# Kernel optimization log

Measured on AMD Instinct MI355X. Metric: run time of the kernel, lower is better.

Reference implementation:

```python
import jax, jax.numpy as jnp
import numpy as np

B, P, H, A = 256, 196, 1024, 512

def setup_inputs() -> dict:
    key = jax.random.key(0)
    ks = jax.random.split(key, 20)
    s = 1.0 / np.sqrt(H)
    sa = 1.0 / np.sqrt(A)
    return {
        "spatial_image": jax.random.normal(ks[0], (B, P, H), jnp.float32),
        "decoder_out": jax.random.normal(ks[1], (B, H), jnp.float32),
        "st": jax.random.normal(ks[2], (B, H), jnp.float32),
        "W_sen_aff": jax.random.uniform(ks[3], (H, H), jnp.float32, -s, s),
        "b_sen_aff": jax.random.uniform(ks[4], (H,), jnp.float32, -s, s),
        "W_sen_att": jax.random.uniform(ks[5], (H, A), jnp.float32, -s, s),
        "b_sen_att": jax.random.uniform(ks[6], (A,), jnp.float32, -s, s),
        "W_h_aff": jax.random.uniform(ks[7], (H, H), jnp.float32, -s, s),
        "b_h_aff": jax.random.uniform(ks[8], (H,), jnp.float32, -s, s),
        "W_h_att": jax.random.uniform(ks[9], (H, A), jnp.float32, -s, s),
        "b_h_att": jax.random.uniform(ks[10], (A,), jnp.float32, -s, s),
        "W_v_att": jax.random.uniform(ks[11], (H, A), jnp.float32, -s, s),
        "b_v_att": jax.random.uniform(ks[12], (A,), jnp.float32, -s, s),
        "W_alpha": jax.random.uniform(ks[13], (A, 1), jnp.float32, -sa, sa),
        "b_alpha": jax.random.uniform(ks[14], (1,), jnp.float32, -sa, sa),
        "W_ctx": jax.random.uniform(ks[15], (H, H), jnp.float32, -s, s),
        "b_ctx": jax.random.uniform(ks[16], (H,), jnp.float32, -s, s),
    }

def reference(spatial_image, decoder_out, st,
              W_sen_aff, b_sen_aff, W_sen_att, b_sen_att,
              W_h_aff, b_h_aff, W_h_att, b_h_att,
              W_v_att, b_v_att, W_alpha, b_alpha, W_ctx, b_ctx):
    # visual_attn: [B, P, A]
    visual_attn = jnp.einsum('bph,ha->bpa', spatial_image, W_v_att) + b_v_att
    # sentinel path: [B, H] -> relu affine -> [B, A]
    sentinel_affine = jax.nn.relu(st @ W_sen_aff + b_sen_aff)
    sentinel_attn = sentinel_affine @ W_sen_att + b_sen_att
    # hidden path: [B, H] -> tanh affine -> [B, A]
    hidden_affine = jnp.tanh(decoder_out @ W_h_aff + b_h_aff)
    hidden_attn = hidden_affine @ W_h_att + b_h_att
    # concat sentinel as an extra "pixel": [B, P+1, H] and [B, P+1, A]
    concat_features = jnp.concatenate([spatial_image, sentinel_affine[:, None, :]], axis=1)
    attended_features = jnp.concatenate([visual_attn, sentinel_attn[:, None, :]], axis=1)
    attention = jnp.tanh(attended_features + hidden_attn[:, None, :])  # [B, P+1, A]
    alpha = (jnp.einsum('bpa,ao->bpo', attention, W_alpha) + b_alpha)[..., 0]  # [B, P+1]
    att_weights = jax.nn.softmax(alpha, axis=1)
    context = jnp.einsum('bph,bp->bh', concat_features, att_weights)  # [B, H]
    beta_value = att_weights[:, -1:]  # [B, 1]
    out_l = jnp.tanh((context + hidden_affine) @ W_ctx + b_ctx)  # [B, H]
    return (out_l, att_weights, beta_value)
```

## Files before the change

### kernel.cpp

```cpp
#include <hip/hip_runtime.h>
#include <hip/hip_bf16.h>
#include <stdint.h>
#include <stddef.h>

typedef __attribute__((ext_vector_type(4))) float f32x4;
typedef __attribute__((ext_vector_type(8))) short short8;

#define MROWS 50176


static __device__ __forceinline__ int lds_off(int row, int k) {
    int slot = (k >> 3) ^ ((row >> 1) & 3);
    return (row << 6) + (slot << 4) + ((k & 7) << 1);
}

static __device__ __forceinline__ unsigned div196(unsigned g) {
    return (unsigned)(((unsigned long long)g * 85599ull) >> 24);
}

static __device__ __forceinline__ unsigned short f2bf(float f) {
    union { float f; unsigned u; } v; v.f = f;
    unsigned r = v.u + 0x7FFFu + ((v.u >> 16) & 1u);
    return (unsigned short)(r >> 16);
}

static __device__ __forceinline__ unsigned long long pack4bf(f32x4 a) {
    union { unsigned long long u; __hip_bfloat162 h[2]; } r;
    r.h[0] = __float22bfloat162_rn(make_float2(a[0], a[1]));
    r.h[1] = __float22bfloat162_rn(make_float2(a[2], a[3]));
    return r.u;
}

static __device__ __forceinline__ float tanh_fast(float x) {
    float xc = fminf(fmaxf(x, -9.f), 9.f);
    float e = __builtin_amdgcn_exp2f(xc * 2.885390081777927f);
    return (e - 1.f) * __builtin_amdgcn_rcpf(e + 1.f);
}

static __device__ __forceinline__ void gload_lds16(const void* g, void* l) {
    __builtin_amdgcn_global_load_lds(
        (const __attribute__((address_space(1))) unsigned int*)g,
        (__attribute__((address_space(3))) unsigned int*)l, 16, 0, 0);
}

template<bool PREF, bool LATE, int VEND>
static __device__ __forceinline__ void pipe_step(
    int t,
    const float* const (&Ap)[4], const int (&aoff)[4],
    const unsigned short* const (&Bp)[2], const int (&bdst)[2],
    char* sAcur, char* sAnxt, char* sB, int bc, int bn,
    f32x4 (&aCon)[4], f32x4 (&aFill)[4], f32x4 (&acc)[4][4],
    int wr, int wc, int lrow, int lk)
{
    char* sBc = sB + (bc << 13);
    if (PREF) {
        char* sBn = sB + (bn << 13);
        const int ko = (t + 2) << 5;
        gload_lds16(Bp[0] + ko, sBn + bdst[0]);
        gload_lds16(Bp[1] + ko, sBn + bdst[1]);
        #pragma unroll
        for (int r = 0; r < 4; ++r) aFill[r] = *(const f32x4*)(Ap[r] + ko);
    }
    short8 af[4], bf[4];
    #pragma unroll
    for (int m = 0; m < 4; ++m)
        af[m] = *(const short8*)(sAcur + lds_off((wr << 6) + (m << 4) + lrow, lk << 3));
    #pragma unroll
    for (int n = 0; n < 4; ++n)
        bf[n] = *(const short8*)(sBc + lds_off((wc << 6) + (n << 4) + lrow, lk << 3));
    __builtin_amdgcn_s_setprio(1);
    #pragma unroll
    for (int m = 0; m < 4; ++m)
        #pragma unroll
        for (int n = 0; n < 4; ++n)
            acc[m][n] = __builtin_amdgcn_mfma_f32_16x16x32_bf16(af[m], bf[n], acc[m][n], 0, 0, 0);
    __builtin_amdgcn_s_setprio(0);
    if (LATE) {
        #pragma unroll
        for (int r = 0; r < 4; ++r)
            *(unsigned long long*)(sAnxt + aoff[r]) = pack4bf(aCon[r]);
        asm volatile("s_waitcnt vmcnt(%0)" :: "n"(VEND) : "memory");
        asm volatile("s_waitcnt lgkmcnt(0)" ::: "memory");
        __builtin_amdgcn_s_barrier();
    }
}

static __device__ __forceinline__ void kloop_pipe(
    const float* __restrict__ Abase,
    const unsigned short* __restrict__ Bbase,
    char* sA, char* sB,
    f32x4 (&acc)[4][4], int tid)
{
    const int lane = tid & 63, w = tid >> 6;
    const int lrow = lane & 15, lk = lane >> 4;
    const int wr = w >> 1, wc = w & 1;

    const float* Ap[4];
    int aoff[4];
    #pragma unroll
    for (int r = 0; r < 4; ++r) {
        int q = tid + (r << 8);
        int ar = q >> 3, kc = (q & 7) << 2;
        Ap[r] = Abase + (size_t)ar * 1024 + kc;
        aoff[r] = lds_off(ar, kc);
    }
    const unsigned short* Bp[2];
    int bdst[2];
    #pragma unroll
    for (int c = 0; c < 2; ++c) {
        int ch = (w << 1) + c;
        int row = (ch << 4) + (lane >> 2);
        int kg = (lane & 3) ^ ((row >> 1) & 3);
        Bp[c] = Bbase + (size_t)row * 1024 + (kg << 3);
        bdst[c] = ch << 10;
    }

    f32x4 z = {0.f, 0.f, 0.f, 0.f};
    #pragma unroll
    for (int m = 0; m < 4; ++m)
        #pragma unroll
        for (int n = 0; n < 4; ++n) acc[m][n] = z;

    f32x4 aX[4], aY[4];

    gload_lds16(Bp[0], sB + bdst[0]);
    gload_lds16(Bp[1], sB + bdst[1]);
    gload_lds16(Bp[0] + 32, sB + 8192 + bdst[0]);
    gload_lds16(Bp[1] + 32, sB + 8192 + bdst[1]);
    #pragma unroll
    for (int r = 0; r < 4; ++r) aX[r] = *(const f32x4*)Ap[r];
    asm volatile("s_waitcnt vmcnt(0)" ::: "memory");
    #pragma unroll
    for (int r = 0; r < 4; ++r)
        *(unsigned long long*)(sA + aoff[r]) = pack4bf(aX[r]);
    #pragma unroll
    for (int r = 0; r < 4; ++r) aY[r] = *(const f32x4*)(Ap[r] + 32);
    asm volatile("s_waitcnt lgkmcnt(0)" ::: "memory");
    __builtin_amdgcn_s_barrier();

    int bc = 0, bn = 2;
    #pragma unroll 1
    for (int t = 0; t < 30; t += 2) {
        pipe_step<true, true, 6>(t, Ap, aoff, Bp, bdst,
            sA, sA + 8192, sB, bc, bn, aY, aX, acc, wr, wc, lrow, lk);
        bc = (bc == 2) ? 0 : bc + 1;  bn = (bn == 2) ? 0 : bn + 1;
        pipe_step<true, true, 6>(t + 1, Ap, aoff, Bp, bdst,
            sA + 8192, sA, sB, bc, bn, aX, aY, acc, wr, wc, lrow, lk);
        bc = (bc == 2) ? 0 : bc + 1;  bn = (bn == 2) ? 0 : bn + 1;
    }
    pipe_step<false, true, 0>(30, Ap, aoff, Bp, bdst,
        sA, sA + 8192, sB, bc, bn, aY, aX, acc, wr, wc, lrow, lk);
    bc = (bc == 2) ? 0 : bc + 1;
    pipe_step<false, false, 0>(31, Ap, aoff, Bp, bdst,
        sA + 8192, sA, sB, bc, bn, aX, aY, acc, wr, wc, lrow, lk);
}

__global__ __launch_bounds__(256, 3) void attn_alpha_kernel(
    const float* __restrict__ spatial,
    const unsigned short* __restrict__ WvT,
    const float* __restrict__ b_v_att,
    const float* __restrict__ hidden_attn,
    const float* __restrict__ W_alpha,
    float* __restrict__ alphap)
{
    __shared__ char sA[2][8192];
    __shared__ char sB[3][8192];
    __shared__ float alpha_s[2][128];
    const int tid = threadIdx.x;
    const int j = blockIdx.x;
    const int wk = (j & 7) * 196 + (j >> 3);
    const int mt = wk >> 2, n4 = wk & 3;
    const int row0 = mt << 7, col0 = n4 << 7;

    f32x4 acc[4][4];
    kloop_pipe(spatial + (size_t)row0 * 1024, WvT + (size_t)col0 * 1024,
               &sA[0][0], &sB[0][0], acc, tid);

    const int lane = tid & 63, w = tid >> 6;
    const int wr = w >> 1, wc = w & 1;
    const int lrow = lane & 15, lk = lane >> 4;

    const unsigned bb0 = div196((unsigned)row0);
    const unsigned bb1 = div196((unsigned)(row0 + 127));
    float bv[4], wa[4], h0[4], h1[4];
    #pragma unroll
    for (int n = 0; n < 4; ++n) {
        int g = col0 + (wc << 6) + (n << 4) + lrow;
        bv[n] = b_v_att[g];
        wa[n] = W_alpha[g];
        h0[n] = hidden_attn[bb0 * 512 + g];
        h1[n] = hidden_attn[bb1 * 512 + g];
    }
    #pragma unroll
    for (int m = 0; m < 4; ++m) {
        #pragma unroll
        for (int i = 0; i < 4; ++i) {
            int rloc = (wr << 6) + (m << 4) + (lk << 2) + i;
            bool first = (div196((unsigned)(row0 + rloc)) == bb0);
            float s = 0.f;
            #pragma unroll
            for (int n = 0; n < 4; ++n) {
                float v = tanh_fast(acc[m][n][i] + bv[n] + (first ? h0[n] : h1[n]));
                s += v * wa[n];
            }
            #pragma unroll
            for (int off = 1; off < 16; off <<= 1) s += __shfl_xor(s, off);
            if (lrow == 0) alpha_s[wc][rloc] = s;
        }
    }
    __syncthreads();
    if (tid < 128)
        alphap[(size_t)n4 * MROWS + row0 + tid] = alpha_s[0][tid] + alpha_s[1][tid];
}

static __device__ __forceinline__ void kloop_dbuf(
    const float* __restrict__ Abase,
    const unsigned short* __restrict__ Bbase,
    char* sA0, char* sA1, char* sB0, char* sB1,
    f32x4 acc[4][4], int tid)
{
    const int lane = tid & 63, w = tid >> 6;
    const int lrow = lane & 15, lk = lane >> 4;
    const int wr = w >> 1, wc = w & 1;

    const float* Ap[4];
    int aoff[4];
    #pragma unroll
    for (int r = 0; r < 4; ++r) {
        int q = tid + (r << 8);
        int ar = q >> 3, kc = (q & 7) << 2;
        Ap[r] = Abase + (size_t)ar * 1024 + kc;
        aoff[r] = lds_off(ar, kc);
    }
    const unsigned short* Bp[2];
    int bdst[2];
    #pragma unroll
    for (int c = 0; c < 2; ++c) {
        int ch = (w << 1) + c;
        int row = (ch << 4) + (lane >> 2);
        int kg = (lane & 3) ^ ((row >> 1) & 3);
        Bp[c] = Bbase + (size_t)row * 1024 + (kg << 3);
        bdst[c] = ch << 10;
    }

    f32x4 z = {0.f, 0.f, 0.f, 0.f};
    #pragma unroll
    for (int m = 0; m < 4; ++m)
        #pragma unroll
        for (int n = 0; n < 4; ++n) acc[m][n] = z;

    {
        f32x4 a[4];
        #pragma unroll
        for (int r = 0; r < 4; ++r) a[r] = *(const f32x4*)Ap[r];
        #pragma unroll
        for (int c = 0; c < 2; ++c) gload_lds16(Bp[c], sB0 + bdst[c]);
        #pragma unroll
        for (int r = 0; r < 4; ++r)
            *(unsigned long long*)(sA0 + aoff[r]) = pack4bf(a[r]);
    }
    __syncthreads();

    char* sAc = sA0; char* sAn = sA1;
    char* sBc = sB0; char* sBn = sB1;
    for (int ks = 0; ks < 32; ++ks) {
        f32x4 an[4];
        if (ks < 31) {
            const int ko = (ks + 1) << 5;
            #pragma unroll
            for (int r = 0; r < 4; ++r) an[r] = *(const f32x4*)(Ap[r] + ko);
            #pragma unroll
            for (int c = 0; c < 2; ++c) gload_lds16(Bp[c] + ko, sBn + bdst[c]);
        }
        short8 af[4], bf[4];
        #pragma unroll
        for (int m = 0; m < 4; ++m)
            af[m] = *(const short8*)(sAc + lds_off((wr << 6) + (m << 4) + lrow, lk << 3));
        #pragma unroll
        for (int n = 0; n < 4; ++n)
            bf[n] = *(const short8*)(sBc + lds_off((wc << 6) + (n << 4) + lrow, lk << 3));
        #pragma unroll
        for (int m = 0; m < 4; ++m)
            #pragma unroll
            for (int n = 0; n < 4; ++n)
                acc[m][n] = __builtin_amdgcn_mfma_f32_16x16x32_bf16(af[m], bf[n], acc[m][n], 0, 0, 0);
        if (ks < 31) {
            #pragma unroll
            for (int r = 0; r < 4; ++r)
                *(unsigned long long*)(sAn + aoff[r]) = pack4bf(an[r]);
        }
        __syncthreads();
        char* t;
        t = sAc; sAc = sAn; sAn = t;
        t = sBc; sBc = sBn; sBn = t;
    }
}

struct GemmDesc { const float* A; const unsigned short* BT; const float* bias; float* C; int N; int act; };
struct GemmPair { GemmDesc d[2]; };

__global__ __launch_bounds__(256, 4) void gemm_pair_kernel(GemmPair p)
{
    GemmDesc d = p.d[blockIdx.z];
    __shared__ char sA[2][8192];
    __shared__ char sB[2][8192];
    const int tid = threadIdx.x;
    const int row0 = blockIdx.x << 7;
    const int col0 = blockIdx.y << 7;
    f32x4 acc[4][4];
    kloop_dbuf(d.A + (size_t)row0 * 1024, d.BT + (size_t)col0 * 1024,
               sA[0], sA[1], sB[0], sB[1], acc, tid);
    const int lane = tid & 63, w = tid >> 6;
    const int wr = w >> 1, wc = w & 1;
    const int lrow = lane & 15, lk = lane >> 4;
    #pragma unroll
    for (int n = 0; n < 4; ++n) {
        int col = col0 + (wc << 6) + (n << 4) + lrow;
        float bs = d.bias[col];
        #pragma unroll
        for (int m = 0; m < 4; ++m) {
            int rbase = row0 + (wr << 6) + (m << 4) + (lk << 2);
            #pragma unroll
            for (int i = 0; i < 4; ++i) {
                float v = acc[m][n][i] + bs;
                if (d.act == 1) v = fmaxf(v, 0.f);
                if (d.act == 2) v = tanh_fast(v);
                d.C[(size_t)(rbase + i) * d.N + col] = v;
            }
        }
    }
}

struct TransDesc { const float* src; unsigned short* dst; int K; int N; };
struct TransArgs { TransDesc d[6]; };

__global__ void transpose_cvt_kernel(TransArgs args) {
    TransDesc d = args.d[blockIdx.y];
    int nt = d.N >> 5;
    int tiles = (d.K >> 5) * nt;
    if ((int)blockIdx.x >= tiles) return;
    int tk = blockIdx.x / nt, tn = blockIdx.x % nt;
    __shared__ unsigned short tile[32][33];
    int tx = threadIdx.x & 31, ty = threadIdx.x >> 5;
    int k0 = tk << 5, n0 = tn << 5;
    #pragma unroll
    for (int j = 0; j < 4; ++j)
        tile[ty + j * 8][tx] = f2bf(d.src[(size_t)(k0 + ty + j * 8) * d.N + n0 + tx]);
    __syncthreads();
    #pragma unroll
    for (int j = 0; j < 4; ++j)
        d.dst[(size_t)(n0 + ty + j * 8) * d.K + k0 + tx] = tile[tx][ty + j * 8];
}

__global__ void softmax_sentinel_kernel(
    const float* __restrict__ alphap,
    const float* __restrict__ sen_att, const float* __restrict__ hid_att,
    const float* __restrict__ W_alpha,
    float* __restrict__ att, float* __restrict__ beta)
{
    int b = blockIdx.x, tid = threadIdx.x;
    __shared__ float al[197];
    __shared__ float red[4];
    if (tid < 196) {
        size_t g = (size_t)b * 196 + tid;
        al[tid] = alphap[g] + alphap[MROWS + g] + alphap[2 * MROWS + g] + alphap[3 * MROWS + g];
    }
    float s = 0.f;
    for (int a = tid; a < 512; a += 256)
        s += tanh_fast(sen_att[b * 512 + a] + hid_att[b * 512 + a]) * W_alpha[a];
    #pragma unroll
    for (int off = 1; off < 64; off <<= 1) s += __shfl_xor(s, off);
    if ((tid & 63) == 0) red[tid >> 6] = s;
    __syncthreads();
    if (tid == 0) al[196] = red[0] + red[1] + red[2] + red[3];
    __syncthreads();
    if (tid < 64) {
        float v[4];
        float mx = -1e30f;
        #pragma unroll
        for (int jj = 0; jj < 4; ++jj) {
            int i = tid + jj * 64;
            v[jj] = (i < 197) ? al[i] : -1e30f;
            mx = fmaxf(mx, v[jj]);
        }
        #pragma unroll
        for (int off = 1; off < 64; off <<= 1) mx = fmaxf(mx, __shfl_xor(mx, off));
        float sm = 0.f;
        #pragma unroll
        for (int jj = 0; jj < 4; ++jj) {
            v[jj] = __builtin_amdgcn_exp2f((v[jj] - mx) * 1.442695040888963f);
            if (tid + jj * 64 >= 197) v[jj] = 0.f;
            sm += v[jj];
        }
        #pragma unroll
        for (int off = 1; off < 64; off <<= 1) sm += __shfl_xor(sm, off);
        float inv = 1.f / sm;
        #pragma unroll
        for (int jj = 0; jj < 4; ++jj) {
            int i = tid + jj * 64;
            if (i < 197) {
                float wv = v[jj] * inv;
                att[b * 197 + i] = wv;
                if (i == 196) beta[b] = wv;
            }
        }
    }
}

__global__ __launch_bounds__(256) void context_kernel(
    const float* __restrict__ spatial, const float* __restrict__ sen_aff,
    const float* __restrict__ hid_aff, const float* __restrict__ att,
    float* __restrict__ ctxh)
{
    int b = blockIdx.x, half = blockIdx.y, t = threadIdx.x;
    __shared__ float wsm[197];
    if (t < 197) wsm[t] = att[b * 197 + t];
    __syncthreads();
    int h2 = (half << 8) + t;
    const float2* sp = (const float2*)(spatial + (size_t)b * 196 * 1024) + h2;
    float ax = 0.f, ay = 0.f;
    #pragma unroll 8
    for (int p = 0; p < 196; ++p) {
        float2 x = sp[(size_t)p * 512];
        ax += wsm[p] * x.x; ay += wsm[p] * x.y;
    }
    float w196 = wsm[196];
    float2 sa = ((const float2*)(sen_aff + (size_t)b * 1024))[h2];
    float2 ha = ((const float2*)(hid_aff + (size_t)b * 1024))[h2];
    ctxh[(size_t)b * 1024 + 2 * h2]     = ax + w196 * sa.x + ha.x;
    ctxh[(size_t)b * 1024 + 2 * h2 + 1] = ay + w196 * sa.y + ha.y;
}

extern "C" void kernel_launch(void* const* d_in, const int* in_sizes, int n_in,
                              void* d_out, int out_size, void* d_ws, size_t ws_size,
                              hipStream_t stream)
{
    const float* spatial   = (const float*)d_in[0];
    const float* decoder   = (const float*)d_in[1];
    const float* st        = (const float*)d_in[2];
    const float* W_sen_aff = (const float*)d_in[3];
    const float* b_sen_aff = (const float*)d_in[4];
    const float* W_sen_att = (const float*)d_in[5];
    const float* b_sen_att = (const float*)d_in[6];
    const float* W_h_aff   = (const float*)d_in[7];
    const float* b_h_aff   = (const float*)d_in[8];
    const float* W_h_att   = (const float*)d_in[9];
    const float* b_h_att   = (const float*)d_in[10];
    const float* W_v_att   = (const float*)d_in[11];
    const float* b_v_att   = (const float*)d_in[12];
    const float* W_alpha   = (const float*)d_in[13];
    const float* W_ctx     = (const float*)d_in[15];
    const float* b_ctx     = (const float*)d_in[16];

    char* ws = (char*)d_ws;
    size_t off = 0;
    auto alloc = [&](size_t bytes) {
        char* p = ws + off; off += (bytes + 255) & ~(size_t)255; return p;
    };
    unsigned short* WvT  = (unsigned short*)alloc((size_t)512 * 1024 * 2);
    unsigned short* WsaT = (unsigned short*)alloc((size_t)1024 * 1024 * 2);
    unsigned short* WstT = (unsigned short*)alloc((size_t)512 * 1024 * 2);
    unsigned short* WhaT = (unsigned short*)alloc((size_t)1024 * 1024 * 2);
    unsigned short* WhtT = (unsigned short*)alloc((size_t)512 * 1024 * 2);
    unsigned short* WcxT = (unsigned short*)alloc((size_t)1024 * 1024 * 2);
    float* sen_aff = (float*)alloc((size_t)256 * 1024 * 4);
    float* sen_att = (float*)alloc((size_t)256 * 512 * 4);
    float* hid_aff = (float*)alloc((size_t)256 * 1024 * 4);
    float* hid_att = (float*)alloc((size_t)256 * 512 * 4);
    float* alphap  = (float*)alloc((size_t)4 * MROWS * 4);
    float* ctxh    = (float*)alloc((size_t)256 * 1024 * 4);

    float* out_l    = (float*)d_out;
    float* out_att  = out_l + 256 * 1024;
    float* out_beta = out_att + 256 * 197;

    TransArgs ta;
    ta.d[0] = { W_v_att,   WvT,  1024, 512  };
    ta.d[1] = { W_sen_aff, WsaT, 1024, 1024 };
    ta.d[2] = { W_sen_att, WstT, 1024, 512  };
    ta.d[3] = { W_h_aff,   WhaT, 1024, 1024 };
    ta.d[4] = { W_h_att,   WhtT, 1024, 512  };
    ta.d[5] = { W_ctx,     WcxT, 1024, 1024 };
    transpose_cvt_kernel<<<dim3(1024, 6), 256, 0, stream>>>(ta);

    GemmPair p1;
    p1.d[0] = { st,      WsaT, b_sen_aff, sen_aff, 1024, 1 };
    p1.d[1] = { decoder, WhaT, b_h_aff,   hid_aff, 1024, 2 };
    gemm_pair_kernel<<<dim3(2, 8, 2), 256, 0, stream>>>(p1);

    GemmPair p2;
    p2.d[0] = { sen_aff, WstT, b_sen_att, sen_att, 512, 0 };
    p2.d[1] = { hid_aff, WhtT, b_h_att,   hid_att, 512, 0 };
    gemm_pair_kernel<<<dim3(2, 4, 2), 256, 0, stream>>>(p2);

    attn_alpha_kernel<<<1568, 256, 0, stream>>>(spatial, WvT, b_v_att, hid_att, W_alpha, alphap);
    softmax_sentinel_kernel<<<256, 256, 0, stream>>>(alphap, sen_att, hid_att, W_alpha, out_att, out_beta);
    context_kernel<<<dim3(256, 2), 256, 0, stream>>>(spatial, sen_aff, hid_aff, out_att, ctxh);

    GemmPair p3;
    p3.d[0] = { ctxh, WcxT, b_ctx, out_l, 1024, 2 };
    p3.d[1] = { ctxh, WcxT, b_ctx, out_l, 1024, 2 };
    gemm_pair_kernel<<<dim3(2, 8, 1), 256, 0, stream>>>(p3);
}
```

Baseline: 224.6 us.

## Pre-convert spatial features to bf16 and reuse them in attention and context

Adds a kernel that converts the whole fp32 spatial tensor to bf16 once. The attention-alpha GEMM then streams both operands straight into LDS with direct global-to-LDS loads in a triple-buffered loop, and the context reduction reads the half-size bf16 copy. It also moves the small GEMMs onto the pipelined K-loop. The extra conversion pass reads the full fp32 tensor and writes a bf16 copy, which costs about as much traffic as the single fp32 read it replaces. The context sum now uses bf16-rounded spatial values, and the path is chosen only when the workspace is large enough.

Result: slower. 400.6 us (+78.4%).

```diff
diff --git a/kernel.cpp b/kernel.cpp
--- a/kernel.cpp
+++ b/kernel.cpp
@@ -22,6 +22,10 @@
     union { float f; unsigned u; } v; v.f = f;
     unsigned r = v.u + 0x7FFFu + ((v.u >> 16) & 1u);
     return (unsigned short)(r >> 16);
+}
+
+static __device__ __forceinline__ float bf2f(unsigned short u) {
+    union { unsigned v; float f; } x; x.v = ((unsigned)u) << 16; return x.f;
 }
 
 static __device__ __forceinline__ unsigned long long pack4bf(f32x4 a) {
@@ -43,50 +47,24 @@
         (__attribute__((address_space(3))) unsigned int*)l, 16, 0, 0);
 }
 
-template<bool PREF, bool LATE, int VEND>
-static __device__ __forceinline__ void pipe_step(
-    int t,
-    const float* const (&Ap)[4], const int (&aoff)[4],
-    const unsigned short* const (&Bp)[2], const int (&bdst)[2],
-    char* sAcur, char* sAnxt, char* sB, int bc, int bn,
-    f32x4 (&aCon)[4], f32x4 (&aFill)[4], f32x4 (&acc)[4][4],
-    int wr, int wc, int lrow, int lk)
-{
-    char* sBc = sB + (bc << 13);
-    if (PREF) {
-        char* sBn = sB + (bn << 13);
-        const int ko = (t + 2) << 5;
-        gload_lds16(Bp[0] + ko, sBn + bdst[0]);
-        gload_lds16(Bp[1] + ko, sBn + bdst[1]);
-        #pragma unroll
-        for (int r = 0; r < 4; ++r) aFill[r] = *(const f32x4*)(Ap[r] + ko);
-    }
-    short8 af[4], bf[4];
-    #pragma unroll
-    for (int m = 0; m < 4; ++m)
-        af[m] = *(const short8*)(sAcur + lds_off((wr << 6) + (m << 4) + lrow, lk << 3));
-    #pragma unroll
-    for (int n = 0; n < 4; ++n)
-        bf[n] = *(const short8*)(sBc + lds_off((wc << 6) + (n << 4) + lrow, lk << 3));
-    __builtin_amdgcn_s_setprio(1);
-    #pragma unroll
-    for (int m = 0; m < 4; ++m)
-        #pragma unroll
-        for (int n = 0; n < 4; ++n)
-            acc[m][n] = __builtin_amdgcn_mfma_f32_16x16x32_bf16(af[m], bf[n], acc[m][n], 0, 0, 0);
-    __builtin_amdgcn_s_setprio(0);
-    if (LATE) {
-        #pragma unroll
-        for (int r = 0; r < 4; ++r)
-            *(unsigned long long*)(sAnxt + aoff[r]) = pack4bf(aCon[r]);
-        asm volatile("s_waitcnt vmcnt(%0)" :: "n"(VEND) : "memory");
-        asm volatile("s_waitcnt lgkmcnt(0)" ::: "memory");
-        __builtin_amdgcn_s_barrier();
-    }
-}
-
-static __device__ __forceinline__ void kloop_pipe(
-    const float* __restrict__ Abase,
+__global__ __launch_bounds__(256) void cvt_spatial_kernel(
+    const float* __restrict__ src, unsigned short* __restrict__ dst)
+{
+    const size_t total = (size_t)MROWS * 1024;
+    size_t i = ((size_t)blockIdx.x * 256 + threadIdx.x) * 8;
+    const size_t stride = (size_t)gridDim.x * 256 * 8;
+    for (; i < total; i += stride) {
+        f32x4 lo = *(const f32x4*)(src + i);
+        f32x4 hi = *(const f32x4*)(src + i + 4);
+        union { short8 s; unsigned long long u[2]; } o;
+        o.u[0] = pack4bf(lo);
+        o.u[1] = pack4bf(hi);
+        *(short8*)(dst + i) = o.s;
+    }
+}
+
+static __device__ __forceinline__ void kloop_sym(
+    const unsigned short* __restrict__ Abase,
     const unsigned short* __restrict__ Bbase,
     char* sA, char* sB,
     f32x4 (&acc)[4][4], int tid)
@@ -95,24 +73,16 @@
     const int lrow = lane & 15, lk = lane >> 4;
     const int wr = w >> 1, wc = w & 1;
 
-    const float* Ap[4];
-    int aoff[4];
-    #pragma unroll
-    for (int r = 0; r < 4; ++r) {
-        int q = tid + (r << 8);
-        int ar = q >> 3, kc = (q & 7) << 2;
-        Ap[r] = Abase + (size_t)ar * 1024 + kc;
-        aoff[r] = lds_off(ar, kc);
-    }
-    const unsigned short* Bp[2];
-    int bdst[2];
+    const unsigned short *Ap[2], *Bp[2];
+    int dst[2];
     #pragma unroll
     for (int c = 0; c < 2; ++c) {
         int ch = (w << 1) + c;
         int row = (ch << 4) + (lane >> 2);
         int kg = (lane & 3) ^ ((row >> 1) & 3);
+        Ap[c] = Abase + (size_t)row * 1024 + (kg << 3);
         Bp[c] = Bbase + (size_t)row * 1024 + (kg << 3);
-        bdst[c] = ch << 10;
+        dst[c] = ch << 10;
     }
 
     f32x4 z = {0.f, 0.f, 0.f, 0.f};
@@ -121,49 +91,63 @@
         #pragma unroll
         for (int n = 0; n < 4; ++n) acc[m][n] = z;
 
-    f32x4 aX[4], aY[4];
-
-    gload_lds16(Bp[0], sB + bdst[0]);
-    gload_lds16(Bp[1], sB + bdst[1]);
-    gload_lds16(Bp[0] + 32, sB + 8192 + bdst[0]);
-    gload_lds16(Bp[1] + 32, sB + 8192 + bdst[1]);
-    #pragma unroll
-    for (int r = 0; r < 4; ++r) aX[r] = *(const f32x4*)Ap[r];
-    asm volatile("s_waitcnt vmcnt(0)" ::: "memory");
-    #pragma unroll
-    for (int r = 0; r < 4; ++r)
-        *(unsigned long long*)(sA + aoff[r]) = pack4bf(aX[r]);
-    #pragma unroll
-    for (int r = 0; r < 4; ++r) aY[r] = *(const f32x4*)(Ap[r] + 32);
-    asm volatile("s_waitcnt lgkmcnt(0)" ::: "memory");
+    #pragma unroll
+    for (int s = 0; s < 2; ++s) {
+        const int ko = s << 5;
+        gload_lds16(Ap[0] + ko, sA + (s << 13) + dst[0]);
+        gload_lds16(Ap[1] + ko, sA + (s << 13) + dst[1]);
+        gload_lds16(Bp[0] + ko, sB + (s << 13) + dst[0]);
+        gload_lds16(Bp[1] + ko, sB + (s << 13) + dst[1]);
+    }
+    asm volatile("s_waitcnt vmcnt(4)" ::: "memory");
     __builtin_amdgcn_s_barrier();
 
-    int bc = 0, bn = 2;
+    char *a0 = sA, *a1 = sA + 8192, *a2 = sA + 16384;
+    char *b0 = sB, *b1 = sB + 8192, *b2 = sB + 16384;
     #pragma unroll 1
-    for (int t = 0; t < 30; t += 2) {
-        pipe_step<true, true, 6>(t, Ap, aoff, Bp, bdst,
-            sA, sA + 8192, sB, bc, bn, aY, aX, acc, wr, wc, lrow, lk);
-        bc = (bc == 2) ? 0 : bc + 1;  bn = (bn == 2) ? 0 : bn + 1;
-        pipe_step<true, true, 6>(t + 1, Ap, aoff, Bp, bdst,
-            sA + 8192, sA, sB, bc, bn, aX, aY, acc, wr, wc, lrow, lk);
-        bc = (bc == 2) ? 0 : bc + 1;  bn = (bn == 2) ? 0 : bn + 1;
-    }
-    pipe_step<false, true, 0>(30, Ap, aoff, Bp, bdst,
-        sA, sA + 8192, sB, bc, bn, aY, aX, acc, wr, wc, lrow, lk);
-    bc = (bc == 2) ? 0 : bc + 1;
-    pipe_step<false, false, 0>(31, Ap, aoff, Bp, bdst,
-        sA + 8192, sA, sB, bc, bn, aX, aY, acc, wr, wc, lrow, lk);
-}
-
-__global__ __launch_bounds__(256, 3) void attn_alpha_kernel(
-    const float* __restrict__ spatial,
+    for (int t = 0; t < 32; ++t) {
+        if (t < 30) {
+            const int ko = (t + 2) << 5;
+            gload_lds16(Ap[0] + ko, a2 + dst[0]);
+            gload_lds16(Ap[1] + ko, a2 + dst[1]);
+            gload_lds16(Bp[0] + ko, b2 + dst[0]);
+            gload_lds16(Bp[1] + ko, b2 + dst[1]);
+        }
+        short8 af[4], bf[4];
+        #pragma unroll
+        for (int m = 0; m < 4; ++m)
+            af[m] = *(const short8*)(a0 + lds_off((wr << 6) + (m << 4) + lrow, lk << 3));
+        #pragma unroll
+        for (int n = 0; n < 4; ++n)
+            bf[n] = *(const short8*)(b0 + lds_off((wc << 6) + (n << 4) + lrow, lk << 3));
+        __builtin_amdgcn_s_setprio(1);
+        #pragma unroll
+        for (int m = 0; m < 4; ++m)
+            #pragma unroll
+            for (int n = 0; n < 4; ++n)
+                acc[m][n] = __builtin_amdgcn_mfma_f32_16x16x32_bf16(af[m], bf[n], acc[m][n], 0, 0, 0);
+        __builtin_amdgcn_s_setprio(0);
+        if (t < 31) {
+            if (t < 30) asm volatile("s_waitcnt vmcnt(4)" ::: "memory");
+            else        asm volatile("s_waitcnt vmcnt(0)" ::: "memory");
+            asm volatile("s_waitcnt lgkmcnt(0)" ::: "memory");
+            __builtin_amdgcn_s_barrier();
+            char* t0;
+            t0 = a0; a0 = a1; a1 = a2; a2 = t0;
+            t0 = b0; b0 = b1; b1 = b2; b2 = t0;
+        }
+    }
+}
+
+__global__ __launch_bounds__(256, 3) void attn_alpha_bf16_kernel(
+    const unsigned short* __restrict__ spat_bf,
     const unsigned short* __restrict__ WvT,
     const float* __restrict__ b_v_att,
     const float* __restrict__ hidden_attn,
     const float* __restrict__ W_alpha,
     float* __restrict__ alphap)
 {
-    __shared__ char sA[2][8192];
+    __shared__ char sA[3][8192];
     __shared__ char sB[3][8192];
     __shared__ float alpha_s[2][128];
     const int tid = threadIdx.x;
@@ -173,8 +157,8 @@
     const int row0 = mt << 7, col0 = n4 << 7;
 
     f32x4 acc[4][4];
-    kloop_pipe(spatial + (size_t)row0 * 1024, WvT + (size_t)col0 * 1024,
-               &sA[0][0], &sB[0][0], acc, tid);
+    kloop_sym(spat_bf + (size_t)row0 * 1024, WvT + (size_t)col0 * 1024,
+              &sA[0][0], &sB[0][0], acc, tid);
 
     const int lane = tid & 63, w = tid >> 6;
     const int wr = w >> 1, wc = w & 1;
@@ -213,11 +197,53 @@
         alphap[(size_t)n4 * MROWS + row0 + tid] = alpha_s[0][tid] + alpha_s[1][tid];
 }
 
-static __device__ __forceinline__ void kloop_dbuf(
+template<bool PREF, bool LATE, int VEND>
+static __device__ __forceinline__ void pipe_step(
+    int t,
+    const float* const (&Ap)[4], const int (&aoff)[4],
+    const unsigned short* const (&Bp)[2], const int (&bdst)[2],
+    char* sAcur, char* sAnxt, char* sB, int bc, int bn,
+    f32x4 (&aCon)[4], f32x4 (&aFill)[4], f32x4 (&acc)[4][4],
+    int wr, int wc, int lrow, int lk)
+{
+    char* sBc = sB + (bc << 13);
+    if (PREF) {
+        char* sBn = sB + (bn << 13);
+        const int ko = (t + 2) << 5;
+        gload_lds16(Bp[0] + ko, sBn + bdst[0]);
+        gload_lds16(Bp[1] + ko, sBn + bdst[1]);
+        #pragma unroll
+        for (int r = 0; r < 4; ++r) aFill[r] = *(const f32x4*)(Ap[r] + ko);
+    }
+    short8 af[4], bf[4];
+    #pragma unroll
+    for (int m = 0; m < 4; ++m)
+        af[m] = *(const short8*)(sAcur + lds_off((wr << 6) + (m << 4) + lrow, lk << 3));
+    #pragma unroll
+    for (int n = 0; n < 4; ++n)
+        bf[n] = *(const short8*)(sBc + lds_off((wc << 6) + (n << 4) + lrow, lk << 3));
+    __builtin_amdgcn_s_setprio(1);
+    #pragma unroll
+    for (int m = 0; m < 4; ++m)
+        #pragma unroll
+        for (int n = 0; n < 4; ++n)
+            acc[m][n] = __builtin_amdgcn_mfma_f32_16x16x32_bf16(af[m], bf[n], acc[m][n], 0, 0, 0);
+    __builtin_amdgcn_s_setprio(0);
+    if (LATE) {
+        #pragma unroll
+        for (int r = 0; r < 4; ++r)
+            *(unsigned long long*)(sAnxt + aoff[r]) = pack4bf(aCon[r]);
+        asm volatile("s_waitcnt vmcnt(%0)" :: "n"(VEND) : "memory");
+        asm volatile("s_waitcnt lgkmcnt(0)" ::: "memory");
+        __builtin_amdgcn_s_barrier();
+    }
+}
+
+static __device__ __forceinline__ void kloop_pipe(
     const float* __restrict__ Abase,
     const unsigned short* __restrict__ Bbase,
-    char* sA0, char* sA1, char* sB0, char* sB1,
-    f32x4 acc[4][4], int tid)
+    char* sA, char* sB,
+    f32x4 (&acc)[4][4], int tid)
 {
     const int lane = tid & 63, w = tid >> 6;
     const int lrow = lane & 15, lk = lane >> 4;
@@ -249,51 +275,96 @@
         #pragma unroll
         for (int n = 0; n < 4; ++n) acc[m][n] = z;
 
-    {
-        f32x4 a[4];
-        #pragma unroll
-        for (int r = 0; r < 4; ++r) a[r] = *(const f32x4*)Ap[r];
-        #pragma unroll
-        for (int c = 0; c < 2; ++c) gload_lds16(Bp[c], sB0 + bdst[c]);
-        #pragma unroll
-        for (int r = 0; r < 4; ++r)
-            *(unsigned long long*)(sA0 + aoff[r]) = pack4bf(a[r]);
+    f32x4 aX[4], aY[4];
+
+    gload_lds16(Bp[0], sB + bdst[0]);
+    gload_lds16(Bp[1], sB + bdst[1]);
+    gload_lds16(Bp[0] + 32, sB + 8192 + bdst[0]);
+    gload_lds16(Bp[1] + 32, sB + 8192 + bdst[1]);
+    #pragma unroll
+    for (int r = 0; r < 4; ++r) aX[r] = *(const f32x4*)Ap[r];
+    asm volatile("s_waitcnt vmcnt(0)" ::: "memory");
+    #pragma unroll
+    for (int r = 0; r < 4; ++r)
+        *(unsigned long long*)(sA + aoff[r]) = pack4bf(aX[r]);
+    #pragma unroll
+    for (int r = 0; r < 4; ++r) aY[r] = *(const f32x4*)(Ap[r] + 32);
+    asm volatile("s_waitcnt lgkmcnt(0)" ::: "memory");
+    __builtin_amdgcn_s_barrier();
+
+    int bc = 0, bn = 2;
+    #pragma unroll 1
+    for (int t = 0; t < 30; t += 2) {
+        pipe_step<true, true, 6>(t, Ap, aoff, Bp, bdst,
+            sA, sA + 8192, sB, bc, bn, aY, aX, acc, wr, wc, lrow, lk);
+        bc = (bc == 2) ? 0 : bc + 1;  bn = (bn == 2) ? 0 : bn + 1;
+        pipe_step<true, true, 6>(t + 1, Ap, aoff, Bp, bdst,
+            sA + 8192, sA, sB, bc, bn, aX, aY, acc, wr, wc, lrow, lk);
+        bc = (bc == 2) ? 0 : bc + 1;  bn = (bn == 2) ? 0 : bn + 1;
+    }
+    pipe_step<false, true, 0>(30, Ap, aoff, Bp, bdst,
+        sA, sA + 8192, sB, bc, bn, aY, aX, acc, wr, wc, lrow, lk);
+    bc = (bc == 2) ? 0 : bc + 1;
+    pipe_step<false, false, 0>(31, Ap, aoff, Bp, bdst,
+        sA + 8192, sA, sB, bc, bn, aX, aY, acc, wr, wc, lrow, lk);
+}
+
+__global__ __launch_bounds__(256, 3) void attn_alpha_f32_kernel(
+    const float* __restrict__ spatial,
+    const unsigned short* __restrict__ WvT,
+    const float* __restrict__ b_v_att,
+    const float* __restrict__ hidden_attn,
+    const float* __restrict__ W_alpha,
+    float* __restrict__ alphap)
+{
+    __shared__ char sA[2][8192];
+    __shared__ char sB[3][8192];
+    __shared__ float alpha_s[2][128];
+    const int tid = threadIdx.x;
+    const int j = blockIdx.x;
+    const int wk = (j & 7) * 196 + (j >> 3);
+    const int mt = wk >> 2, n4 = wk & 3;
+    const int row0 = mt << 7, col0 = n4 << 7;
+
+    f32x4 acc[4][4];
+    kloop_pipe(spatial + (size_t)row0 * 1024, WvT + (size_t)col0 * 1024,
+               &sA[0][0], &sB[0][0], acc, tid);
+
+    const int lane = tid & 63, w = tid >> 6;
+    const int wr = w >> 1, wc = w & 1;
+    const int lrow = lane & 15, lk = lane >> 4;
+
+    const unsigned bb0 = div196((unsigned)row0);
+    const unsigned bb1 = div196((unsigned)(row0 + 127));
+    float bv[4], wa[4], h0[4], h1[4];
+    #pragma unroll
+    for (int n = 0; n < 4; ++n) {
+        int g = col0 + (wc << 6) + (n << 4) + lrow;
+        bv[n] = b_v_att[g];
+        wa[n] = W_alpha[g];
+        h0[n] = hidden_attn[bb0 * 512 + g];
+        h1[n] = hidden_attn[bb1 * 512 + g];
+    }
+    #pragma unroll
+    for (int m = 0; m < 4; ++m) {
+        #pragma unroll
+        for (int i = 0; i < 4; ++i) {
+            int rloc = (wr << 6) + (m << 4) + (lk << 2) + i;
+            bool first = (div196((unsigned)(row0 + rloc)) == bb0);
+            float s = 0.f;
+            #pragma unroll
+            for (int n = 0; n < 4; ++n) {
+                float v = tanh_fast(acc[m][n][i] + bv[n] + (first ? h0[n] : h1[n]));
+                s += v * wa[n];
+            }
+            #pragma unroll
+            for (int off = 1; off < 16; off <<= 1) s += __shfl_xor(s, off);
+            if (lrow == 0) alpha_s[wc][rloc] = s;
+        }
     }
     __syncthreads();
-
-    char* sAc = sA0; char* sAn = sA1;
-    char* sBc = sB0; char* sBn = sB1;
-    for (int ks = 0; ks < 32; ++ks) {
-        f32x4 an[4];
-        if (ks < 31) {
-            const int ko = (ks + 1) << 5;
-            #pragma unroll
-            for (int r = 0; r < 4; ++r) an[r] = *(const f32x4*)(Ap[r] + ko);
-            #pragma unroll
-            for (int c = 0; c < 2; ++c) gload_lds16(Bp[c] + ko, sBn + bdst[c]);
-        }
-        short8 af[4], bf[4];
-        #pragma unroll
-        for (int m = 0; m < 4; ++m)
-            af[m] = *(const short8*)(sAc + lds_off((wr << 6) + (m << 4) + lrow, lk << 3));
-        #pragma unroll
-        for (int n = 0; n < 4; ++n)
-            bf[n] = *(const short8*)(sBc + lds_off((wc << 6) + (n << 4) + lrow, lk << 3));
-        #pragma unroll
-        for (int m = 0; m < 4; ++m)
-            #pragma unroll
-            for (int n = 0; n < 4; ++n)
-                acc[m][n] = __builtin_amdgcn_mfma_f32_16x16x32_bf16(af[m], bf[n], acc[m][n], 0, 0, 0);
-        if (ks < 31) {
-            #pragma unroll
-            for (int r = 0; r < 4; ++r)
-                *(unsigned long long*)(sAn + aoff[r]) = pack4bf(an[r]);
-        }
-        __syncthreads();
-        char* t;
-        t = sAc; sAc = sAn; sAn = t;
-        t = sBc; sBc = sBn; sBn = t;
-    }
+    if (tid < 128)
+        alphap[(size_t)n4 * MROWS + row0 + tid] = alpha_s[0][tid] + alpha_s[1][tid];
 }
 
 struct GemmDesc { const float* A; const unsigned short* BT; const float* bias; float* C; int N; int act; };
@@ -303,13 +374,13 @@
 {
     GemmDesc d = p.d[blockIdx.z];
     __shared__ char sA[2][8192];
-    __shared__ char sB[2][8192];
+    __shared__ char sB[3][8192];
     const int tid = threadIdx.x;
     const int row0 = blockIdx.x << 7;
     const int col0 = blockIdx.y << 7;
     f32x4 acc[4][4];
-    kloop_dbuf(d.A + (size_t)row0 * 1024, d.BT + (size_t)col0 * 1024,
-               sA[0], sA[1], sB[0], sB[1], acc, tid);
+    kloop_pipe(d.A + (size_t)row0 * 1024, d.BT + (size_t)col0 * 1024,
+               &sA[0][0], &sB[0][0], acc, tid);
     const int lane = tid & 63, w = tid >> 6;
     const int wr = w >> 1, wc = w & 1;
     const int lrow = lane & 15, lk = lane >> 4;
@@ -407,7 +478,38 @@
     }
 }
 
-__global__ __launch_bounds__(256) void context_kernel(
+__global__ __launch_bounds__(256) void context_bf16_kernel(
+    const unsigned short* __restrict__ spat_bf, const float* __restrict__ sen_aff,
+    const float* __restrict__ hid_aff, const float* __restrict__ att,
+    float* __restrict__ ctxh)
+{
+    int b = blockIdx.x, t = threadIdx.x;
+    __shared__ float wsm[197];
+    if (t < 197) wsm[t] = att[b * 197 + t];
+    __syncthreads();
+    const unsigned short* sp = spat_bf + (size_t)b * 196 * 1024 + (t << 2);
+    float a0 = 0.f, a1 = 0.f, a2 = 0.f, a3 = 0.f;
+    #pragma unroll 4
+    for (int p = 0; p < 196; ++p) {
+        unsigned long long x = *(const unsigned long long*)(sp + (size_t)p * 1024);
+        float wv = wsm[p];
+        a0 += wv * bf2f((unsigned short)x);
+        a1 += wv * bf2f((unsigned short)(x >> 16));
+        a2 += wv * bf2f((unsigned short)(x >> 32));
+        a3 += wv * bf2f((unsigned short)(x >> 48));
+    }
+    float w196 = wsm[196];
+    f32x4 sa = ((const f32x4*)(sen_aff + (size_t)b * 1024))[t];
+    f32x4 ha = ((const f32x4*)(hid_aff + (size_t)b * 1024))[t];
+    f32x4 o;
+    o[0] = a0 + w196 * sa[0] + ha[0];
+    o[1] = a1 + w196 * sa[1] + ha[1];
+    o[2] = a2 + w196 * sa[2] + ha[2];
+    o[3] = a3 + w196 * sa[3] + ha[3];
+    ((f32x4*)(ctxh + (size_t)b * 1024))[t] = o;
+}
+
+__global__ __launch_bounds__(256) void context_f32_kernel(
     const float* __restrict__ spatial, const float* __restrict__ sen_aff,
     const float* __restrict__ hid_aff, const float* __restrict__ att,
     float* __restrict__ ctxh)
@@ -470,9 +572,16 @@
     float* alphap  = (float*)alloc((size_t)4 * MROWS * 4);
     float* ctxh    = (float*)alloc((size_t)256 * 1024 * 4);
 
+    const size_t spat_bytes = (size_t)MROWS * 1024 * 2;
+    unsigned short* spat_bf = (unsigned short*)(ws + off);
+    const bool bigws = (off + spat_bytes) <= ws_size;
+
     float* out_l    = (float*)d_out;
     float* out_att  = out_l + 256 * 1024;
     float* out_beta = out_att + 256 * 197;
+
+    if (bigws)
+        cvt_spatial_kernel<<<2048, 256, 0, stream>>>(spatial, spat_bf);
 
     TransArgs ta;
     ta.d[0] = { W_v_att,   WvT,  1024, 512  };
@@ -493,9 +602,17 @@
     p2.d[1] = { hid_aff, WhtT, b_h_att,   hid_att, 512, 0 };
     gemm_pair_kernel<<<dim3(2, 4, 2), 256, 0, stream>>>(p2);
 
-    attn_alpha_kernel<<<1568, 256, 0, stream>>>(spatial, WvT, b_v_att, hid_att, W_alpha, alphap);
+    if (bigws)
+        attn_alpha_bf16_kernel<<<1568, 256, 0, stream>>>(spat_bf, WvT, b_v_att, hid_att, W_alpha, alphap);
+    else
+        attn_alpha_f32_kernel<<<1568, 256, 0, stream>>>(spatial, WvT, b_v_att, hid_att, W_alpha, alphap);
+
     softmax_sentinel_kernel<<<256, 256, 0, stream>>>(alphap, sen_att, hid_att, W_alpha, out_att, out_beta);
-    context_kernel<<<dim3(256, 2), 256, 0, stream>>>(spatial, sen_aff, hid_aff, out_att, ctxh);
+
+    if (bigws)
+        context_bf16_kernel<<<256, 256, 0, stream>>>(spat_bf, sen_aff, hid_aff, out_att, ctxh);
+    else
+        context_f32_kernel<<<dim3(256, 2), 256, 0, stream>>>(spatial, sen_aff, hid_aff, out_att, ctxh);
 
     GemmPair p3;
     p3.d[0] = { ctxh, WcxT, b_ctx, out_l, 1024, 2 };
```

## Deepen GEMM k-loop prefetch pipeline from two to three stages ahead

Applied to the files above, without the earlier changes.

Restructures the visual-attention GEMM main loop so that global loads for the A (fp32 activations) and B (bf16 weights) tiles are issued three k-steps ahead instead of two. It uses four LDS buffers for B and three register sets for A, rotated each step, with vmcnt waits adjusted to match. The goal is to hide more global memory latency behind the MFMA work. In exchange it adds 8 KB of LDS and more live registers, which could reduce occupancy at the launch bound of 3 blocks per CU.

New measurement: 354.6 us. 57.9% more time.

```diff
diff --git a/kernel.cpp b/kernel.cpp
--- a/kernel.cpp
+++ b/kernel.cpp
@@ -43,23 +43,21 @@
         (__attribute__((address_space(3))) unsigned int*)l, 16, 0, 0);
 }
 
-template<bool PREF, bool LATE, int VEND>
-static __device__ __forceinline__ void pipe_step(
+template<int VEND, bool ISSUE>
+static __device__ __forceinline__ void pipe3_step(
     int t,
     const float* const (&Ap)[4], const int (&aoff)[4],
     const unsigned short* const (&Bp)[2], const int (&bdst)[2],
-    char* sAcur, char* sAnxt, char* sB, int bc, int bn,
-    f32x4 (&aCon)[4], f32x4 (&aFill)[4], f32x4 (&acc)[4][4],
+    char* sAcur, char* sAnxt, char* pRead, char* pIssue,
+    f32x4 (&setI)[4], f32x4 (&setW)[4], f32x4 (&acc)[4][4],
     int wr, int wc, int lrow, int lk)
 {
-    char* sBc = sB + (bc << 13);
-    if (PREF) {
-        char* sBn = sB + (bn << 13);
-        const int ko = (t + 2) << 5;
-        gload_lds16(Bp[0] + ko, sBn + bdst[0]);
-        gload_lds16(Bp[1] + ko, sBn + bdst[1]);
-        #pragma unroll
-        for (int r = 0; r < 4; ++r) aFill[r] = *(const f32x4*)(Ap[r] + ko);
+    if (ISSUE) {
+        const int ko = (t + 3) << 5;
+        gload_lds16(Bp[0] + ko, pIssue + bdst[0]);
+        gload_lds16(Bp[1] + ko, pIssue + bdst[1]);
+        #pragma unroll
+        for (int r = 0; r < 4; ++r) setI[r] = *(const f32x4*)(Ap[r] + ko);
     }
     short8 af[4], bf[4];
     #pragma unroll
@@ -67,7 +65,7 @@
         af[m] = *(const short8*)(sAcur + lds_off((wr << 6) + (m << 4) + lrow, lk << 3));
     #pragma unroll
     for (int n = 0; n < 4; ++n)
-        bf[n] = *(const short8*)(sBc + lds_off((wc << 6) + (n << 4) + lrow, lk << 3));
+        bf[n] = *(const short8*)(pRead + lds_off((wc << 6) + (n << 4) + lrow, lk << 3));
     __builtin_amdgcn_s_setprio(1);
     #pragma unroll
     for (int m = 0; m < 4; ++m)
@@ -75,85 +73,16 @@
         for (int n = 0; n < 4; ++n)
             acc[m][n] = __builtin_amdgcn_mfma_f32_16x16x32_bf16(af[m], bf[n], acc[m][n], 0, 0, 0);
     __builtin_amdgcn_s_setprio(0);
-    if (LATE) {
-        #pragma unroll
-        for (int r = 0; r < 4; ++r)
-            *(unsigned long long*)(sAnxt + aoff[r]) = pack4bf(aCon[r]);
-        asm volatile("s_waitcnt vmcnt(%0)" :: "n"(VEND) : "memory");
-        asm volatile("s_waitcnt lgkmcnt(0)" ::: "memory");
-        __builtin_amdgcn_s_barrier();
-    }
-}
-
-static __device__ __forceinline__ void kloop_pipe(
-    const float* __restrict__ Abase,
-    const unsigned short* __restrict__ Bbase,
-    char* sA, char* sB,
-    f32x4 (&acc)[4][4], int tid)
-{
-    const int lane = tid & 63, w = tid >> 6;
-    const int lrow = lane & 15, lk = lane >> 4;
-    const int wr = w >> 1, wc = w & 1;
-
-    const float* Ap[4];
-    int aoff[4];
-    #pragma unroll
-    for (int r = 0; r < 4; ++r) {
-        int q = tid + (r << 8);
-        int ar = q >> 3, kc = (q & 7) << 2;
-        Ap[r] = Abase + (size_t)ar * 1024 + kc;
-        aoff[r] = lds_off(ar, kc);
-    }
-    const unsigned short* Bp[2];
-    int bdst[2];
-    #pragma unroll
-    for (int c = 0; c < 2; ++c) {
-        int ch = (w << 1) + c;
-        int row = (ch << 4) + (lane >> 2);
-        int kg = (lane & 3) ^ ((row >> 1) & 3);
-        Bp[c] = Bbase + (size_t)row * 1024 + (kg << 3);
-        bdst[c] = ch << 10;
-    }
-
-    f32x4 z = {0.f, 0.f, 0.f, 0.f};
-    #pragma unroll
-    for (int m = 0; m < 4; ++m)
-        #pragma unroll
-        for (int n = 0; n < 4; ++n) acc[m][n] = z;
-
-    f32x4 aX[4], aY[4];
-
-    gload_lds16(Bp[0], sB + bdst[0]);
-    gload_lds16(Bp[1], sB + bdst[1]);
-    gload_lds16(Bp[0] + 32, sB + 8192 + bdst[0]);
-    gload_lds16(Bp[1] + 32, sB + 8192 + bdst[1]);
-    #pragma unroll
-    for (int r = 0; r < 4; ++r) aX[r] = *(const f32x4*)Ap[r];
-    asm volatile("s_waitcnt vmcnt(0)" ::: "memory");
     #pragma unroll
     for (int r = 0; r < 4; ++r)
-        *(unsigned long long*)(sA + aoff[r]) = pack4bf(aX[r]);
-    #pragma unroll
-    for (int r = 0; r < 4; ++r) aY[r] = *(const f32x4*)(Ap[r] + 32);
+        *(unsigned long long*)(sAnxt + aoff[r]) = pack4bf(setW[r]);
+    asm volatile("s_waitcnt vmcnt(%0)" :: "n"(VEND) : "memory");
     asm volatile("s_waitcnt lgkmcnt(0)" ::: "memory");
     __builtin_amdgcn_s_barrier();
-
-    int bc = 0, bn = 2;
-    #pragma unroll 1
-    for (int t = 0; t < 30; t += 2) {
-        pipe_step<true, true, 6>(t, Ap, aoff, Bp, bdst,
-            sA, sA + 8192, sB, bc, bn, aY, aX, acc, wr, wc, lrow, lk);
-        bc = (bc == 2) ? 0 : bc + 1;  bn = (bn == 2) ? 0 : bn + 1;
-        pipe_step<true, true, 6>(t + 1, Ap, aoff, Bp, bdst,
-            sA + 8192, sA, sB, bc, bn, aX, aY, acc, wr, wc, lrow, lk);
-        bc = (bc == 2) ? 0 : bc + 1;  bn = (bn == 2) ? 0 : bn + 1;
-    }
-    pipe_step<false, true, 0>(30, Ap, aoff, Bp, bdst,
-        sA, sA + 8192, sB, bc, bn, aY, aX, acc, wr, wc, lrow, lk);
-    bc = (bc == 2) ? 0 : bc + 1;
-    pipe_step<false, false, 0>(31, Ap, aoff, Bp, bdst,
-        sA + 8192, sA, sB, bc, bn, aX, aY, acc, wr, wc, lrow, lk);
-}
+}
+
+#define ROT4() { char* _t = qa; qa = qb; qb = qc; qc = qd; qd = _t; \
+                 _t = ca; ca = cb; cb = _t; }
 
 __global__ __launch_bounds__(256, 3) void attn_alpha_kernel(
     const float* __restrict__ spatial,
@@ -164,7 +93,7 @@
     float* __restrict__ alphap)
 {
     __shared__ char sA[2][8192];
-    __shared__ char sB[3][8192];
+    __shared__ char sB[4][8192];
     __shared__ float alpha_s[2][128];
     const int tid = threadIdx.x;
     const int j = blockIdx.x;
@@ -172,13 +101,93 @@
     const int mt = wk >> 2, n4 = wk & 3;
     const int row0 = mt << 7, col0 = n4 << 7;
 
+    const int lane = tid & 63, w = tid >> 6;
+    const int lrow = lane & 15, lk = lane >> 4;
+    const int wr = w >> 1, wc = w & 1;
+
+    const float* Abase = spatial + (size_t)row0 * 1024;
+    const unsigned short* Bbase = WvT + (size_t)col0 * 1024;
+
+    const float* Ap[4];
+    int aoff[4];
+    #pragma unroll
+    for (int r = 0; r < 4; ++r) {
+        int q = tid + (r << 8);
+        int ar = q >> 3, kc = (q & 7) << 2;
+        Ap[r] = Abase + (size_t)ar * 1024 + kc;
+        aoff[r] = lds_off(ar, kc);
+    }
+    const unsigned short* Bp[2];
+    int bdst[2];
+    #pragma unroll
+    for (int c = 0; c < 2; ++c) {
+        int ch = (w << 1) + c;
+        int row = (ch << 4) + (lane >> 2);
+        int kg = (lane & 3) ^ ((row >> 1) & 3);
+        Bp[c] = Bbase + (size_t)row * 1024 + (kg << 3);
+        bdst[c] = ch << 10;
+    }
+
     f32x4 acc[4][4];
-    kloop_pipe(spatial + (size_t)row0 * 1024, WvT + (size_t)col0 * 1024,
-               &sA[0][0], &sB[0][0], acc, tid);
-
-    const int lane = tid & 63, w = tid >> 6;
-    const int wr = w >> 1, wc = w & 1;
-    const int lrow = lane & 15, lk = lane >> 4;
+    f32x4 z = {0.f, 0.f, 0.f, 0.f};
+    #pragma unroll
+    for (int m = 0; m < 4; ++m)
+        #pragma unroll
+        for (int n = 0; n < 4; ++n) acc[m][n] = z;
+
+    char* qa = &sB[0][0]; char* qb = &sB[1][0];
+    char* qc = &sB[2][0]; char* qd = &sB[3][0];
+    char* ca = &sA[0][0]; char* cb = &sA[1][0];
+
+    f32x4 aS0[4], aS1[4], aS2[4];
+
+    #pragma unroll
+    for (int r = 0; r < 4; ++r) aS0[r] = *(const f32x4*)Ap[r];
+    gload_lds16(Bp[0], qa + bdst[0]);
+    gload_lds16(Bp[1], qa + bdst[1]);
+    gload_lds16(Bp[0] + 32, qb + bdst[0]);
+    gload_lds16(Bp[1] + 32, qb + bdst[1]);
+    gload_lds16(Bp[0] + 64, qc + bdst[0]);
+    gload_lds16(Bp[1] + 64, qc + bdst[1]);
+    asm volatile("s_waitcnt vmcnt(4)" ::: "memory");
+    #pragma unroll
+    for (int r = 0; r < 4; ++r)
+        *(unsigned long long*)(ca + aoff[r]) = pack4bf(aS0[r]);
+    #pragma unroll
+    for (int r = 0; r < 4; ++r) aS2[r] = *(const f32x4*)(Ap[r] + 64);
+    #pragma unroll
+    for (int r = 0; r < 4; ++r) aS1[r] = *(const f32x4*)(Ap[r] + 32);
+    asm volatile("s_waitcnt lgkmcnt(0)" ::: "memory");
+    __builtin_amdgcn_s_barrier();
+
+    pipe3_step<6 , true>(0, Ap, aoff, Bp, bdst, ca, cb, qa, qd, aS0, aS1, acc, wr, wc, lrow, lk); ROT4();
+    pipe3_step<12, true>(1, Ap, aoff, Bp, bdst, ca, cb, qa, qd, aS1, aS2, acc, wr, wc, lrow, lk); ROT4();
+    pipe3_step<12, true>(2, Ap, aoff, Bp, bdst, ca, cb, qa, qd, aS2, aS0, acc, wr, wc, lrow, lk); ROT4();
+    #pragma unroll 1
+    for (int g = 1; g < 9; ++g) {
+        const int tb = g * 3;
+        pipe3_step<12, true>(tb    , Ap, aoff, Bp, bdst, ca, cb, qa, qd, aS0, aS1, acc, wr, wc, lrow, lk); ROT4();
+        pipe3_step<12, true>(tb + 1, Ap, aoff, Bp, bdst, ca, cb, qa, qd, aS1, aS2, acc, wr, wc, lrow, lk); ROT4();
+        pipe3_step<12, true>(tb + 2, Ap, aoff, Bp, bdst, ca, cb, qa, qd, aS2, aS0, acc, wr, wc, lrow, lk); ROT4();
+    }
+    pipe3_step<12, true >(27, Ap, aoff, Bp, bdst, ca, cb, qa, qd, aS0, aS1, acc, wr, wc, lrow, lk); ROT4();
+    pipe3_step<12, true >(28, Ap, aoff, Bp, bdst, ca, cb, qa, qd, aS1, aS2, acc, wr, wc, lrow, lk); ROT4();
+    pipe3_step<6 , false>(29, Ap, aoff, Bp, bdst, ca, cb, qa, qd, aS2, aS0, acc, wr, wc, lrow, lk); ROT4();
+    pipe3_step<0 , false>(30, Ap, aoff, Bp, bdst, ca, cb, qa, qd, aS2, aS1, acc, wr, wc, lrow, lk); ROT4();
+    {
+        short8 af[4], bf[4];
+        #pragma unroll
+        for (int m = 0; m < 4; ++m)
+            af[m] = *(const short8*)(ca + lds_off((wr << 6) + (m << 4) + lrow, lk << 3));
+        #pragma unroll
+        for (int n = 0; n < 4; ++n)
+            bf[n] = *(const short8*)(qa + lds_off((wc << 6) + (n << 4) + lrow, lk << 3));
+        #pragma unroll
+        for (int m = 0; m < 4; ++m)
+            #pragma unroll
+            for (int n = 0; n < 4; ++n)
+                acc[m][n] = __builtin_amdgcn_mfma_f32_16x16x32_bf16(af[m], bf[n], acc[m][n], 0, 0, 0);
+    }
 
     const unsigned bb0 = div196((unsigned)row0);
     const unsigned bb1 = div196((unsigned)(row0 + 127));
```
